# Performance work log

Hardware: AMD Instinct MI355X
Metric: run time of the kernel (lower is better)

## Reference

```python
import jax, jax.numpy as jnp
import numpy as np

B, L = 128, 64000
FS, STEP, NFILT, HID, HID2, OUT = 256, 200, 64, 512, 512, 10


def _ilin(lb, ub, W, b=0.0):
    # interval affine: center/radius form
    c = (lb + ub) * 0.5
    r = (ub - lb) * 0.5
    oc = c @ W + b
    orr = r @ jnp.abs(W)
    return oc - orr, oc + orr


def _imul(al, au, bl, bu):
    # interval product: extremes over 4 corner products
    p = jnp.stack([al * bl, al * bu, au * bl, au * bu])
    return p.min(axis=0), p.max(axis=0)


def _cell(xl, xu, hl, hu, cl, cu, wih, whh, bias):
    # interval LSTM cell, torch gate order i,f,g,o
    gl1, gu1 = _ilin(xl, xu, wih)
    gl2, gu2 = _ilin(hl, hu, whh)
    gl = gl1 + gl2 + bias
    gu = gu1 + gu2 + bias
    il, fl, ggl, ol = jnp.split(gl, 4, axis=-1)
    iu, fu, ggu, ou = jnp.split(gu, 4, axis=-1)
    il, iu = jax.nn.sigmoid(il), jax.nn.sigmoid(iu)
    fl, fu = jax.nn.sigmoid(fl), jax.nn.sigmoid(fu)
    ggl, ggu = jnp.tanh(ggl), jnp.tanh(ggu)
    fcl, fcu = _imul(fl, fu, cl, cu)
    igl, igu = _imul(il, iu, ggl, ggu)
    ncl, ncu = fcl + igl, fcu + igu
    nhl, nhu = _imul(jax.nn.sigmoid(ol), jax.nn.sigmoid(ou), jnp.tanh(ncl), jnp.tanh(ncu))
    return nhl, nhu, ncl, ncu


def setup_inputs() -> dict:
    key = jax.random.key(0)
    ks = jax.random.split(key, 13)
    x = 0.1 * jax.random.normal(ks[0], (B, L), jnp.float32)
    eps = 0.01
    s = 0.3  # keep LSTM gates out of saturation
    return {
        "input_lb": x - eps,
        "input_ub": x + eps,
        "mtx1": jax.random.normal(ks[1], (FS, FS + 2), jnp.float32) / np.float32(np.sqrt(FS)),
        "mtx2": jax.random.uniform(ks[2], (FS + 2, NFILT), jnp.float32) / np.float32(FS + 2),
        "lin1_w": jax.random.normal(ks[3], (NFILT, HID), jnp.float32) / np.float32(np.sqrt(NFILT)),
        "lin1_b": 0.01 * jax.random.normal(ks[4], (HID,), jnp.float32),
        "w_ih0": s * jax.random.normal(ks[5], (HID, 4 * HID2), jnp.float32) / np.float32(np.sqrt(HID)),
        "w_hh0": s * jax.random.normal(ks[6], (HID2, 4 * HID2), jnp.float32) / np.float32(np.sqrt(HID2)),
        "b0": 0.01 * jax.random.normal(ks[7], (4 * HID2,), jnp.float32),
        "w_ih1": s * jax.random.normal(ks[8], (HID2, 4 * HID2), jnp.float32) / np.float32(np.sqrt(HID2)),
        "w_hh1": s * jax.random.normal(ks[9], (HID2, 4 * HID2), jnp.float32) / np.float32(np.sqrt(HID2)),
        "b1": 0.01 * jax.random.normal(ks[10], (4 * HID2,), jnp.float32),
        "lin2_w": jax.random.normal(ks[11], (HID2, OUT), jnp.float32) / np.float32(np.sqrt(HID2)),
        "lin2_b": 0.01 * jax.random.normal(ks[12], (OUT,), jnp.float32),
    }


def reference(input_lb, input_ub, mtx1, mtx2, lin1_w, lin1_b,
              w_ih0, w_hh0, b0, w_ih1, w_hh1, b1, lin2_w, lin2_b):
    Bc, Lc = input_lb.shape
    pad = jnp.zeros((Bc, STEP), input_lb.dtype)
    lb = jnp.concatenate([input_lb, pad], axis=1)
    ub = jnp.concatenate([input_ub, pad], axis=1)
    Lp = Lc + STEP
    F = (Lp - FS - 1) // STEP + 1  # frames with i + FS < Lp (break condition)
    idx = jnp.arange(F)[:, None] * STEP + jnp.arange(FS)[None, :]  # [F, FS]
    flb, fub = lb[:, idx], ub[:, idx]  # [B, F, FS]
    # pre-LSTM interval chain, vectorized over all frames
    l1l, l1u = _ilin(flb, fub, mtx1)  # [B, F, FS+2]
    a, b = l1l * l1l, l1u * l1u
    squ = jnp.maximum(a, b)
    sql = jnp.where((l1l <= 0) & (l1u >= 0), 0.0, jnp.minimum(a, b))
    l2l, l2u = _ilin(sql, squ, mtx2, 1e-10)  # mtx2 >= 0, inputs >= 0 -> lb > 0
    lgl, lgu = jnp.log(l2l), jnp.log(l2u)
    n1l, n1u = _ilin(lgl, lgu, lin1_w, lin1_b)  # [B, F, HID]
    rl, ru = jnp.maximum(n1l, 0.0), jnp.maximum(n1u, 0.0)

    H2 = w_hh0.shape[0]
    z = jnp.zeros((Bc, H2), input_lb.dtype)

    def step(carry, xs):
        h0l, h0u, c0l, c0u, h1l, h1u, c1l, c1u = carry
        xl, xu = xs
        h0l, h0u, c0l, c0u = _cell(xl, xu, h0l, h0u, c0l, c0u, w_ih0, w_hh0, b0)
        h1l, h1u, c1l, c1u = _cell(h0l, h0u, h1l, h1u, c1l, c1u, w_ih1, w_hh1, b1)
        return (h0l, h0u, c0l, c0u, h1l, h1u, c1l, c1u), None

    carry, _ = jax.lax.scan(step, (z,) * 8,
                            (jnp.swapaxes(rl, 0, 1), jnp.swapaxes(ru, 0, 1)))
    h1l, h1u = carry[4], carry[5]  # last frame, top LSTM layer
    ol, ou = _ilin(h1l, h1u, lin2_w, lin2_b)
    return jnp.stack([ol, ou])  # [2, B, OUT] logit bounds
```

## Files before the change

kernel.cpp:

```cpp
#include <hip/hip_runtime.h>
#include <hip/hip_bf16.h>
#include <math.h>

#define BATCH 128
#define LEN   64000
#define FS    256
#define STEPS 200
#define NFILT 64
#define HID   512
#define HID2  512
#define NOUT  10
#define NF    320
#define G4    2048
#define KTOT  1024
#define NBLK  256
#define HSLOT (BATCH * HID2)

typedef __bf16  bf16x8 __attribute__((ext_vector_type(8)));
typedef float   f32x4  __attribute__((ext_vector_type(4)));
typedef __hip_bfloat16 hbf;

#define ARV(b)  (128 + (b) * 16)
#define REL_(i) (128 + 4096 + (i) * 16)
#define BAR_WORDS (128 + 4096 + 128)

__device__ __forceinline__ float fsig(float x) { return 1.f / (1.f + __expf(-x)); }
__device__ __forceinline__ float ftanh(float x) { return 1.f - 2.f / (__expf(2.f * x) + 1.f); }
__device__ __forceinline__ void imulf_(float al, float au, float bl, float bu,
                                       float& lo, float& hi) {
    const float p1 = al * bl, p2 = al * bu, p3 = au * bl, p4 = au * bu;
    lo = fminf(fminf(p1, p2), fminf(p3, p4));
    hi = fmaxf(fmaxf(p1, p2), fmaxf(p3, p4));
}

__device__ __forceinline__ bf16x8 loadA16_agent(const hbf* p) {
    union { unsigned long long u[2]; bf16x8 v; } t;
    unsigned long long* q = (unsigned long long*)p;
    t.u[0] = __hip_atomic_load(q,     __ATOMIC_RELAXED, __HIP_MEMORY_SCOPE_AGENT);
    t.u[1] = __hip_atomic_load(q + 1, __ATOMIC_RELAXED, __HIP_MEMORY_SCOPE_AGENT);
    return t.v;
}
__device__ __forceinline__ unsigned ld_flag(const unsigned* p) {
    return __hip_atomic_load(p, __ATOMIC_RELAXED, __HIP_MEMORY_SCOPE_AGENT);
}
__device__ __forceinline__ void st_flag(unsigned* p, unsigned v) {
    __hip_atomic_store(p, v, __ATOMIC_RELAXED, __HIP_MEMORY_SCOPE_AGENT);
}

__global__ __launch_bounds__(256) void prep_weights_kernel(
    const float* __restrict__ wih, const float* __restrict__ whh,
    hbf* __restrict__ Wt)
{
    __shared__ float tile[32][33];
    const int n0 = blockIdx.x * 32;
    const int k0 = blockIdx.y * 32;
    const int tx = threadIdx.x & 31;
    const int ty = threadIdx.x >> 5;

    for (int r = ty; r < 32; r += 8) {
        const int k = k0 + r;
        const float* src = (k < HID) ? (wih + (size_t)k * G4)
                                     : (whh + (size_t)(k - HID) * G4);
        tile[r][tx] = src[n0 + tx];
    }
    __syncthreads();
    for (int r = ty; r < 32; r += 8) {
        const int n = n0 + r;
        Wt[(size_t)n * KTOT + k0 + tx] = __float2bfloat16(tile[tx][r]);
    }
}

__global__ __launch_bounds__(256) void prep_mtx1_kernel(
    const float* __restrict__ mtx1, hbf* __restrict__ W)
{
    __shared__ float tile[32][33];
    const int n0 = blockIdx.x * 32;
    const int k0 = blockIdx.y * 32;
    const int tx = threadIdx.x & 31;
    const int ty = threadIdx.x >> 5;

    for (int r = ty; r < 32; r += 8) {
        const int k = k0 + r;
        const int n = n0 + tx;
        tile[r][tx] = (n < FS + 2) ? mtx1[k * (FS + 2) + n] : 0.f;
    }
    __syncthreads();
    for (int r = ty; r < 32; r += 8) {
        const int n = n0 + r;
        if (n < 272)
            W[(size_t)n * 256 + k0 + tx] = __float2bfloat16(tile[tx][r]);
    }
}

#define FB_A1   0
#define FB_OUT1 35840
#define FB_S2   0
#define FB_S3   35840
#define FB_SIZE 70656

__global__ __launch_bounds__(256) void frontend2_kernel(
    const float* __restrict__ lb, const float* __restrict__ ub,
    const hbf* __restrict__ Wt1f,
    const float* __restrict__ mtx2,
    const float* __restrict__ lin1_w, const float* __restrict__ lin1_b,
    hbf* __restrict__ Xc, hbf* __restrict__ Xr)
{
    __shared__ char fbuf[FB_SIZE];
    hbf*   A1c = (hbf*)(fbuf + FB_A1);
    hbf*   A1r = (hbf*)(fbuf + FB_A1 + 16 * 264 * 2);
    float* o1C = (float*)(fbuf + FB_OUT1);
    float* o1R = (float*)(fbuf + FB_OUT1 + 16 * 272 * 4);
    float* s2c = (float*)(fbuf + FB_S2);
    float* s2r = (float*)(fbuf + FB_S2 + 16 * 258 * 4);
    float* s3c = (float*)(fbuf + FB_S3);
    float* s3r = (float*)(fbuf + FB_S3 + 16 * 64 * 4);

    const int tid = threadIdx.x;
    const int row0 = blockIdx.x * 16;

    for (int c = tid; c < 16 * 256; c += 256) {
        const int m = c >> 8, i = c & 255;
        const int rowid = row0 + m;
        const int f = rowid % NF, b = rowid / NF;
        const int pos = f * STEPS + i;
        float l = 0.f, u = 0.f;
        if (pos < LEN) {
            l = lb[(size_t)b * LEN + pos];
            u = ub[(size_t)b * LEN + pos];
        }
        A1c[m * 264 + i] = __float2bfloat16(0.5f * (l + u));
        A1r[m * 264 + i] = __float2bfloat16(0.5f * (u - l));
    }
    __syncthreads();

    {
        const int w    = tid >> 6;
        const int lane = tid & 63;
        const int op   = w & 1;
        const int nh   = w >> 1;
        const int rc   = lane & 15;
        const int gk   = lane >> 4;
        const unsigned amask = op ? 0x7FFF7FFFu : 0xFFFFFFFFu;
        const hbf* ap = (op ? A1r : A1c) + rc * 264 + 8 * gk;
        float* outp = op ? o1R : o1C;

        for (int nt = nh * 9; nt < nh * 8 + 9; ++nt) {
            f32x4 acc = {0.f, 0.f, 0.f, 0.f};
            const hbf* bp = Wt1f + (size_t)(nt * 16 + rc) * 256 + 8 * gk;
#pragma unroll
            for (int k0 = 0; k0 < 256; k0 += 32) {
                const bf16x8 afr = *(const bf16x8*)(ap + k0);
                union { bf16x8 v; unsigned u[4]; } t2;
                t2.v = *(const bf16x8*)(bp + k0);
                t2.u[0] &= amask; t2.u[1] &= amask;
                t2.u[2] &= amask; t2.u[3] &= amask;
                acc = __builtin_amdgcn_mfma_f32_16x16x32_bf16(afr, t2.v, acc, 0, 0, 0);
            }
            const int n = nt * 16 + rc;
#pragma unroll
            for (int reg = 0; reg < 4; ++reg)
                outp[(4 * gk + reg) * 272 + n] = acc[reg];
        }
    }
    __syncthreads();

    for (int c = tid; c < 16 * 258; c += 256) {
        const int m = c / 258, n = c - m * 258;
        const float oc = o1C[m * 272 + n];
        const float orr = o1R[m * 272 + n];
        const float l1l = oc - orr, l1u = oc + orr;
        const float a = l1l * l1l, bb = l1u * l1u;
        const float squ = fmaxf(a, bb);
        const float sql = (l1l <= 0.f && l1u >= 0.f) ? 0.f : fminf(a, bb);
        s2c[m * 258 + n] = 0.5f * (sql + squ);
        s2r[m * 258 + n] = 0.5f * (squ - sql);
    }
    __syncthreads();

    for (int idx = tid; idx < 16 * 64; idx += 256) {
        const int m = idx >> 6, n = idx & 63;
        float oc = 1e-10f, orr = 0.f;
#pragma unroll 4
        for (int i = 0; i < FS + 2; ++i) {
            const float w = mtx2[i * NFILT + n];
            oc  = fmaf(s2c[m * 258 + i], w, oc);
            orr = fmaf(s2r[m * 258 + i], fabsf(w), orr);
        }
        const float lgl = logf(oc - orr);
        const float lgu = logf(oc + orr);
        s3c[m * 64 + n] = 0.5f * (lgl + lgu);
        s3r[m * 64 + n] = 0.5f * (lgu - lgl);
    }
    __syncthreads();

    for (int idx = tid; idx < 16 * 512; idx += 256) {
        const int m = idx >> 9, j = idx & 511;
        float oc = lin1_b[j], orr = 0.f;
#pragma unroll 4
        for (int i = 0; i < NFILT; ++i) {
            const float w = lin1_w[i * HID + j];
            oc  = fmaf(s3c[m * 64 + i], w, oc);
            orr = fmaf(s3r[m * 64 + i], fabsf(w), orr);
        }
        const float n1l = oc - orr, n1u = oc + orr;
        const float rl = fmaxf(n1l, 0.f), ru = fmaxf(n1u, 0.f);
        const int rowid = row0 + m;
        const int f = rowid % NF, b = rowid / NF;
        const size_t o = ((size_t)f * BATCH + b) * HID + j;
        Xc[o] = __float2bfloat16(0.5f * (rl + ru));
        Xr[o] = __float2bfloat16(0.5f * (ru - rl));
    }
}

__device__ __forceinline__ void gbar(unsigned* bar, unsigned gen,
                                     int bid, int tid) {
    __builtin_amdgcn_s_waitcnt(0);
    __syncthreads();
    if (bid == 0) {
        if (tid != 0) {
            while (ld_flag(&bar[ARV(tid)]) < gen)
                __builtin_amdgcn_s_sleep(1);
        }
        __syncthreads();
        if (tid < 8) st_flag(&bar[REL_(tid)], gen);
    } else {
        if (tid == 0) {
            st_flag(&bar[ARV(bid)], gen);
            while (ld_flag(&bar[REL_(bid & 7)]) < gen)
                __builtin_amdgcn_s_sleep(4);
        }
        asm volatile("" ::: "memory");
    }
    __syncthreads();
}

__device__ __forceinline__ void cell_elem(
    const float C[4], const float R[4], const float bs[4],
    float& cl_r, float& cu_r, float& nhl, float& nhu)
{
    float gl[4], gu[4];
#pragma unroll
    for (int g = 0; g < 4; ++g) {
        gl[g] = C[g] - R[g] + bs[g];
        gu[g] = C[g] + R[g] + bs[g];
    }
    const float il = fsig(gl[0]), iu = fsig(gu[0]);
    const float fl = fsig(gl[1]), fu = fsig(gu[1]);
    const float ggl = ftanh(gl[2]), ggu = ftanh(gu[2]);
    const float ol = fsig(gl[3]), ou = fsig(gu[3]);

    float fcl, fcu, igl, igu;
    imulf_(fl, fu, cl_r, cu_r, fcl, fcu);
    imulf_(il, iu, ggl, ggu, igl, igu);
    const float ncl = fcl + igl, ncu = fcu + igu;
    cl_r = ncl; cu_r = ncu;
    imulf_(ol, ou, ftanh(ncl), ftanh(ncu), nhl, nhu);
}

#define GEMM_HALF(KBASE, MASKED)                                               \
    _Pragma("unroll")                                                          \
    for (int kk = 0; kk < 16; ++kk) {                                          \
        const int KK = (KBASE) + kk;                                           \
        _Pragma("unroll")                                                      \
        for (int g = 0; g < 4; ++g) {                                          \
            union { bf16x8 v; unsigned u[4]; } t2;                             \
            t2.v = *(const bf16x8*)&Wlds[(size_t)(((g << 5) | KK) * 64 + lane) * 8]; \
            if (MASKED) {                                                      \
                t2.u[0] &= 0x7FFF7FFFu; t2.u[1] &= 0x7FFF7FFFu;                \
                t2.u[2] &= 0x7FFF7FFFu; t2.u[3] &= 0x7FFF7FFFu;                \
            }                                                                  \
            acc[g] = __builtin_amdgcn_mfma_f32_16x16x32_bf16(af[kk], t2.v, acc[g], 0, 0, 0); \
        }                                                                      \
    }

#define LOADA16(PTR)                                                           \
    _Pragma("unroll")                                                          \
    for (int i = 0; i < 16; ++i) af[i] = *(const bf16x8*)((PTR) + 32 * i);

#define POLL_GROUP(BASE, TGT)                                                  \
    if (tid < 64) {                                                            \
        const unsigned* pp = &lflags[((BASE) + (tid & 31)) * 16];              \
        for (;;) {                                                             \
            const unsigned v = ld_flag(pp);                                    \
            if (__all((int)v >= (TGT))) break;                                 \
            __builtin_amdgcn_s_sleep(1);                                       \
        }                                                                      \
    }                                                                          \
    __syncthreads();

__global__ __launch_bounds__(256, 1) void lstm_persistent(
    const hbf* Xc, const hbf* Xr,
    hbf* Ring1C, hbf* Ring1R,
    const hbf* __restrict__ Wt0, const hbf* __restrict__ Wt1,
    const float* __restrict__ b0, const float* __restrict__ b1,
    hbf* __restrict__ Ring0C, hbf* __restrict__ Ring0R,
    const hbf* __restrict__ Zbuf,
    hbf* __restrict__ H1c0, hbf* __restrict__ H1r0,
    hbf* __restrict__ H1c1, hbf* __restrict__ H1r1,
    float* __restrict__ h1l, float* __restrict__ h1u,
    unsigned* __restrict__ bar, unsigned* __restrict__ tkt,
    unsigned* __restrict__ lflags)
{
    const int tid = threadIdx.x;
    const int bid = blockIdx.x;

    __shared__ unsigned s_info, s_map;
    __shared__ int s_fast;
    __shared__ hbf   Wlds[4 * 32 * 64 * 8];
    __shared__ float red[2][2][4][64][4];
    __shared__ unsigned short houtC[32][16], houtR[32][16];

    if (tid == 0) {
        unsigned xcc;
        asm volatile("s_getreg_b32 %0, hwreg(HW_REG_XCC_ID)" : "=s"(xcc));
        xcc &= 7u;
        const unsigned slot = __hip_atomic_fetch_add(
            &tkt[xcc * 16], 1u, __ATOMIC_RELAXED, __HIP_MEMORY_SCOPE_AGENT);
        s_info = (xcc << 16) | slot;
    }
    gbar(bar, 1, bid, tid);
    if (tid == 0) {
        unsigned cnt[8]; bool ok = true;
        for (int y = 0; y < 8; ++y) {
            cnt[y] = ld_flag(&tkt[y * 16]);
            ok = ok && (cnt[y] == 32u);
        }
        const unsigned xcc = s_info >> 16, slot = s_info & 0xffffu;
        unsigned rank;
        if (ok) rank = xcc * 32u + slot;
        else { rank = slot; for (unsigned y = 0; y < xcc; ++y) rank += cnt[y]; }
        s_map = rank; s_fast = ok ? 1 : 0;
    }
    __syncthreads();

    const unsigned rank = s_map;
    const bool fast = (s_fast != 0);
    int layer, mgrp, jslot;
    if (fast) { layer = (rank >> 5) & 1; mgrp = rank >> 6; jslot = rank & 31; }
    else      { layer = rank >> 7; mgrp = (rank >> 5) & 3; jslot = rank & 31; }
    const int m0 = mgrp * 32;
    const int j0 = jslot * 16;
    const int lfbase  = layer * 128 + mgrp * 32;
    const int l0fbase = mgrp * 32;
    const int myLf = lfbase + jslot;

    {
        const hbf* Wt = layer ? Wt1 : Wt0;
        for (int c = tid; c < 8192; c += 256) {
            const int g  = c >> 11;
            const int kk = (c >> 6) & 31;
            const int l6 = c & 63;
            const int n  = g * HID2 + j0 + (l6 & 15);
            const int k  = kk * 32 + (l6 >> 4) * 8;
            *(ulonglong2*)&Wlds[(size_t)c * 8] =
                *(const ulonglong2*)(Wt + (size_t)n * KTOT + k);
        }
    }

    const int w    = tid >> 6;
    const int lane = tid & 63;
    const int op   = w & 1;
    const int mh   = w >> 1;
    const int rc   = lane & 15;
    const int gk   = lane >> 4;
    const int aoff = (m0 + mh * 16 + rc) * 512 + 8 * gk;

    hbf* H1cb[2] = { H1c0, H1c1 };
    hbf* H1rb[2] = { H1r0, H1r1 };

    const int mm  = tid >> 4;
    const int cj  = tid & 15;
    const int ll  = ((mm >> 2) << 4) | cj;
    const int rr  = mm & 3;
    const int idx0 = (m0 + mm) * HID2 + j0 + cj;
    const int idx1 = idx0 + 16 * HID2;
    const float* bias = layer ? b1 : b0;
    float bs[4];
#pragma unroll
    for (int g = 0; g < 4; ++g) bs[g] = bias[g * HID2 + j0 + cj];

    const int st_arr = tid >> 7;
    const int st_row = (tid >> 2) & 31;
    const int st_q   = tid & 3;
    const size_t st_off = (size_t)(m0 + st_row) * 512 + j0 + st_q * 4;

    float cAl = 0.f, cAu = 0.f, cBl = 0.f, cBu = 0.f;

    __syncthreads();

    bf16x8 xf[16];
    if (layer == 0) {
        const hbf* p = (op ? Xr : Xc) + aoff;
        bf16x8* af = xf;
        LOADA16(p)
    }

    for (int t = 0; t < NF; ++t) {
        const int wslot = t & 1, rslot = wslot ^ 1;
        f32x4 acc[4] = {f32x4{0,0,0,0}, f32x4{0,0,0,0},
                        f32x4{0,0,0,0}, f32x4{0,0,0,0}};

        if (layer == 0) {
            {
                bf16x8* af = xf;
                if (op) { GEMM_HALF(0, 1) } else { GEMM_HALF(0, 0) }
                const int tn = (t + 1 < NF) ? (t + 1) : t;
                const hbf* p = (op ? Xr : Xc) + (size_t)tn * HSLOT + aoff;
                LOADA16(p)
            }
            POLL_GROUP(lfbase, t)
            {
                const int pt = (t == 0) ? NF : t - 1;
                const hbf* p = (op ? Ring0R : Ring0C) + (size_t)pt * HSLOT + aoff;
                bf16x8 af[16];
                LOADA16(p)
                if (op) { GEMM_HALF(16, 1) } else { GEMM_HALF(16, 0) }
            }
        } else {
            POLL_GROUP(lfbase, t)
            {
                bf16x8 af[16];
                if (fast) {
                    const hbf* p = (t == 0) ? (Zbuf + aoff)
                        : ((op ? (const hbf*)Ring1R : (const hbf*)Ring1C)
                           + (size_t)(t - 1) * HSLOT + aoff);
                    LOADA16(p)
                } else {
                    const hbf* p = (op ? H1rb[rslot] : H1cb[rslot]) + aoff;
#pragma unroll
                    for (int i = 0; i < 16; ++i) af[i] = loadA16_agent(p + 32 * i);
                }
                if (op) { GEMM_HALF(16, 1) } else { GEMM_HALF(16, 0) }
            }
            POLL_GROUP(l0fbase, t + 1)
            {
                const hbf* p = (op ? Ring0R : Ring0C) + (size_t)t * HSLOT + aoff;
                bf16x8 af[16];
                LOADA16(p)
                if (op) { GEMM_HALF(0, 1) } else { GEMM_HALF(0, 0) }
            }
        }

#pragma unroll
        for (int g = 0; g < 4; ++g)
            *((f32x4*)&red[op][mh][g][lane][0]) = acc[g];
        __syncthreads();

        {
            float C0[4], R0[4], C1[4], R1[4];
#pragma unroll
            for (int g = 0; g < 4; ++g) {
                C0[g] = red[0][0][g][ll][rr];
                R0[g] = red[1][0][g][ll][rr];
                C1[g] = red[0][1][g][ll][rr];
                R1[g] = red[1][1][g][ll][rr];
            }
            const bool writeF = (layer == 1) && (t == NF - 1);

            float nhl, nhu;
            cell_elem(C0, R0, bs, cAl, cAu, nhl, nhu);
            {
                const __hip_bfloat16 hc = __float2bfloat16(0.5f * (nhl + nhu));
                const __hip_bfloat16 hr = __float2bfloat16(0.5f * (nhu - nhl));
                houtC[mm][cj] = *(const unsigned short*)&hc;
                houtR[mm][cj] = *(const unsigned short*)&hr;
            }
            if (writeF) { h1l[idx0] = nhl; h1u[idx0] = nhu; }

            cell_elem(C1, R1, bs, cBl, cBu, nhl, nhu);
            {
                const __hip_bfloat16 hc = __float2bfloat16(0.5f * (nhl + nhu));
                const __hip_bfloat16 hr = __float2bfloat16(0.5f * (nhu - nhl));
                houtC[mm + 16][cj] = *(const unsigned short*)&hc;
                houtR[mm + 16][cj] = *(const unsigned short*)&hr;
            }
            if (writeF) { h1l[idx1] = nhl; h1u[idx1] = nhu; }
        }
        __syncthreads();

        {
            hbf *dstC, *dstR;
            if (layer == 0) {
                dstC = Ring0C + (size_t)t * HSLOT;
                dstR = Ring0R + (size_t)t * HSLOT;
            } else if (fast) {
                dstC = Ring1C + (size_t)t * HSLOT;
                dstR = Ring1R + (size_t)t * HSLOT;
            } else {
                dstC = H1cb[wslot];
                dstR = H1rb[wslot];
            }
            const unsigned long long* src = (const unsigned long long*)
                &(st_arr ? houtR : houtC)[st_row][st_q * 4];
            unsigned long long* dst = (unsigned long long*)
                ((st_arr ? dstR : dstC) + st_off);
            __hip_atomic_store(dst, *src, __ATOMIC_RELAXED,
                               __HIP_MEMORY_SCOPE_AGENT);
        }

        __builtin_amdgcn_s_waitcnt(0);
        __syncthreads();
        if (tid == 0)
            st_flag(&lflags[myLf * 16], (unsigned)(t + 1));
    }
}

__global__ __launch_bounds__(64) void final_kernel(
    const float* __restrict__ h1l, const float* __restrict__ h1u,
    const float* __restrict__ w, const float* __restrict__ bias,
    float* __restrict__ out)
{
    const int b = blockIdx.x;
    const int j = threadIdx.x;
    if (j < NOUT) {
        float oc = bias[j], orr = 0.f;
        for (int i = 0; i < HID2; ++i) {
            const float lo = h1l[(size_t)b * HID2 + i];
            const float hi = h1u[(size_t)b * HID2 + i];
            const float wv = w[i * NOUT + j];
            oc  = fmaf(0.5f * (lo + hi), wv, oc);
            orr = fmaf(0.5f * (hi - lo), fabsf(wv), orr);
        }
        out[b * NOUT + j] = oc - orr;
        out[BATCH * NOUT + b * NOUT + j] = oc + orr;
    }
}

extern "C" void kernel_launch(void* const* d_in, const int* in_sizes, int n_in,
                              void* d_out, int out_size, void* d_ws, size_t ws_size,
                              hipStream_t stream)
{
    const float* input_lb = (const float*)d_in[0];
    const float* input_ub = (const float*)d_in[1];
    const float* mtx1     = (const float*)d_in[2];
    const float* mtx2     = (const float*)d_in[3];
    const float* lin1_w   = (const float*)d_in[4];
    const float* lin1_b   = (const float*)d_in[5];
    const float* w_ih0    = (const float*)d_in[6];
    const float* w_hh0    = (const float*)d_in[7];
    const float* b0       = (const float*)d_in[8];
    const float* w_ih1    = (const float*)d_in[9];
    const float* w_hh1    = (const float*)d_in[10];
    const float* b1       = (const float*)d_in[11];
    const float* lin2_w   = (const float*)d_in[12];
    const float* lin2_b   = (const float*)d_in[13];
    float* out = (float*)d_out;

    char* ws = (char*)d_ws;
    size_t off = 0;
    hbf* Xc = (hbf*)(ws + off); off += (size_t)NF * HSLOT * 2;
    hbf* Xr = (hbf*)(ws + off); off += (size_t)NF * HSLOT * 2;
    hbf* Wt0 = (hbf*)(ws + off); off += (size_t)G4 * KTOT * 2;
    hbf* Wt1 = (hbf*)(ws + off); off += (size_t)G4 * KTOT * 2;
    hbf* Wt1f = (hbf*)(ws + off); off += (size_t)272 * 256 * 2;
    hbf* Ring0C = (hbf*)(ws + off); off += (size_t)(NF + 1) * HSLOT * 2;
    hbf* Ring0R = (hbf*)(ws + off); off += (size_t)(NF + 1) * HSLOT * 2;

    char* zbase = ws + off;
    hbf* Zbuf = (hbf*)(ws + off); off += (size_t)HSLOT * 2;
    hbf* H1c0 = (hbf*)(ws + off); off += (size_t)HSLOT * 2;
    hbf* H1r0 = (hbf*)(ws + off); off += (size_t)HSLOT * 2;
    hbf* H1c1 = (hbf*)(ws + off); off += (size_t)HSLOT * 2;
    hbf* H1r1 = (hbf*)(ws + off); off += (size_t)HSLOT * 2;
    unsigned* lflags = (unsigned*)(ws + off); off += (size_t)256 * 16 * 4;
    unsigned* tkt    = (unsigned*)(ws + off); off += (size_t)8 * 16 * 4;
    unsigned* bar    = (unsigned*)(ws + off); off += (size_t)BAR_WORDS * 4;
    const size_t zbytes = (size_t)((ws + off) - zbase);
    float* h1l = (float*)(ws + off); off += (size_t)HSLOT * 4;
    float* h1u = (float*)(ws + off); off += (size_t)HSLOT * 4;

    hipMemsetAsync(zbase, 0, zbytes, stream);
    hipMemsetAsync(Ring0C + (size_t)NF * HSLOT, 0, (size_t)HSLOT * 2, stream);
    hipMemsetAsync(Ring0R + (size_t)NF * HSLOT, 0, (size_t)HSLOT * 2, stream);

    {
        const dim3 pgrid(G4 / 32, KTOT / 32);
        prep_weights_kernel<<<pgrid, 256, 0, stream>>>(w_ih0, w_hh0, Wt0);
        prep_weights_kernel<<<pgrid, 256, 0, stream>>>(w_ih1, w_hh1, Wt1);
        prep_mtx1_kernel<<<dim3(9, 8), 256, 0, stream>>>(mtx1, Wt1f);
    }

    frontend2_kernel<<<(BATCH * NF) / 16, 256, 0, stream>>>(
        input_lb, input_ub, Wt1f, mtx2, lin1_w, lin1_b, Xc, Xr);

    lstm_persistent<<<NBLK, 256, 0, stream>>>(
        Xc, Xr, Xc, Xr, Wt0, Wt1, b0, b1,
        Ring0C, Ring0R, Zbuf,
        H1c0, H1r0, H1c1, H1r1,
        h1l, h1u, bar, tkt, lflags);

    final_kernel<<<BATCH, 64, 0, stream>>>(h1l, h1u, lin2_w, lin2_b, out);
}
```

Before: 3.448 ms.

## Move lin1 interval matmul to MFMA and restructure frontend with 512 threads

Replaces the scalar FMA loop for the lin1 interval affine layer with bf16 MFMA tiles, using a new prep kernel that transposes lin1_w to bf16. The block size goes from 256 to 512 threads, the mtx2 stage computes lower and upper bounds directly (mtx2 is nonnegative) from bf16 squared bounds, and shared memory is compacted. The aim is to cut scalar ALU time in the frontend, at the cost of bf16 precision loss in the squared values and log-feature intermediates.

```diff
diff --git a/kernel.cpp b/kernel.cpp
--- a/kernel.cpp
+++ b/kernel.cpp
@@ -92,44 +92,63 @@
     }
 }
 
-#define FB_A1   0
-#define FB_OUT1 35840
-#define FB_S2   0
-#define FB_S3   35840
-#define FB_SIZE 70656
-
-__global__ __launch_bounds__(256) void frontend2_kernel(
+__global__ __launch_bounds__(256) void prep_lin1_kernel(
+    const float* __restrict__ lin1_w, hbf* __restrict__ W)
+{
+    __shared__ float tile[32][33];
+    const int n0 = blockIdx.x * 32;
+    const int k0 = blockIdx.y * 32;
+    const int tx = threadIdx.x & 31;
+    const int ty = threadIdx.x >> 5;
+
+    for (int r = ty; r < 32; r += 8)
+        tile[r][tx] = lin1_w[(size_t)(k0 + r) * HID + n0 + tx];
+    __syncthreads();
+    for (int r = ty; r < 32; r += 8)
+        W[(size_t)(n0 + r) * 64 + k0 + tx] = __float2bfloat16(tile[tx][r]);
+}
+
+#define FB_A1C  0
+#define FB_A1R  8704
+#define FB_O1C  17408
+#define FB_O1R  34816
+#define FB_S3C  52224
+#define FB_S3R  54272
+#define FB_SIZE 56320
+
+__global__ __launch_bounds__(512) void frontend3_kernel(
     const float* __restrict__ lb, const float* __restrict__ ub,
     const hbf* __restrict__ Wt1f,
     const float* __restrict__ mtx2,
-    const float* __restrict__ lin1_w, const float* __restrict__ lin1_b,
+    const hbf* __restrict__ Wt3f,
+    const float* __restrict__ lin1_b,
     hbf* __restrict__ Xc, hbf* __restrict__ Xr)
 {
     __shared__ char fbuf[FB_SIZE];
-    hbf*   A1c = (hbf*)(fbuf + FB_A1);
-    hbf*   A1r = (hbf*)(fbuf + FB_A1 + 16 * 264 * 2);
-    float* o1C = (float*)(fbuf + FB_OUT1);
-    float* o1R = (float*)(fbuf + FB_OUT1 + 16 * 272 * 4);
-    float* s2c = (float*)(fbuf + FB_S2);
-    float* s2r = (float*)(fbuf + FB_S2 + 16 * 258 * 4);
-    float* s3c = (float*)(fbuf + FB_S3);
-    float* s3r = (float*)(fbuf + FB_S3 + 16 * 64 * 4);
-
-    const int tid = threadIdx.x;
+    hbf*   A1c = (hbf*)(fbuf + FB_A1C);
+    hbf*   A1r = (hbf*)(fbuf + FB_A1R);
+    float* o1C = (float*)(fbuf + FB_O1C);
+    float* o1R = (float*)(fbuf + FB_O1R);
+    hbf*   SQL = A1c;
+    hbf*   SQU = A1r;
+    hbf*   s3c = (hbf*)(fbuf + FB_S3C);
+    hbf*   s3r = (hbf*)(fbuf + FB_S3R);
+
+    const int tid  = threadIdx.x;
     const int row0 = blockIdx.x * 16;
-
-    for (int c = tid; c < 16 * 256; c += 256) {
+    const int b    = row0 / NF;
+    const int f0   = row0 % NF;
+
+    for (int c = tid; c < 16 * 256; c += 512) {
         const int m = c >> 8, i = c & 255;
-        const int rowid = row0 + m;
-        const int f = rowid % NF, b = rowid / NF;
-        const int pos = f * STEPS + i;
+        const int pos = (f0 + m) * STEPS + i;
         float l = 0.f, u = 0.f;
         if (pos < LEN) {
             l = lb[(size_t)b * LEN + pos];
             u = ub[(size_t)b * LEN + pos];
         }
-        A1c[m * 264 + i] = __float2bfloat16(0.5f * (l + u));
-        A1r[m * 264 + i] = __float2bfloat16(0.5f * (u - l));
+        A1c[m * 272 + i] = __float2bfloat16(0.5f * (l + u));
+        A1r[m * 272 + i] = __float2bfloat16(0.5f * (u - l));
     }
     __syncthreads();
 
@@ -141,10 +160,11 @@
         const int rc   = lane & 15;
         const int gk   = lane >> 4;
         const unsigned amask = op ? 0x7FFF7FFFu : 0xFFFFFFFFu;
-        const hbf* ap = (op ? A1r : A1c) + rc * 264 + 8 * gk;
+        const hbf* ap = (op ? A1r : A1c) + rc * 272 + 8 * gk;
         float* outp = op ? o1R : o1C;
-
-        for (int nt = nh * 9; nt < nh * 8 + 9; ++nt) {
+        const int nt0 = nh * 4, nt1 = (nh == 3) ? 17 : nh * 4 + 4;
+
+        for (int nt = nt0; nt < nt1; ++nt) {
             f32x4 acc = {0.f, 0.f, 0.f, 0.f};
             const hbf* bp = Wt1f + (size_t)(nt * 16 + rc) * 256 + 8 * gk;
 #pragma unroll
@@ -164,7 +184,7 @@
     }
     __syncthreads();
 
-    for (int c = tid; c < 16 * 258; c += 256) {
+    for (int c = tid; c < 16 * 258; c += 512) {
         const int m = c / 258, n = c - m * 258;
         const float oc = o1C[m * 272 + n];
         const float orr = o1R[m * 272 + n];
@@ -172,43 +192,65 @@
         const float a = l1l * l1l, bb = l1u * l1u;
         const float squ = fmaxf(a, bb);
         const float sql = (l1l <= 0.f && l1u >= 0.f) ? 0.f : fminf(a, bb);
-        s2c[m * 258 + n] = 0.5f * (sql + squ);
-        s2r[m * 258 + n] = 0.5f * (squ - sql);
-    }
-    __syncthreads();
-
-    for (int idx = tid; idx < 16 * 64; idx += 256) {
+        SQL[m * 272 + n] = __float2bfloat16(sql);
+        SQU[m * 272 + n] = __float2bfloat16(squ);
+    }
+    __syncthreads();
+
+    for (int idx = tid; idx < 16 * 64; idx += 512) {
         const int m = idx >> 6, n = idx & 63;
-        float oc = 1e-10f, orr = 0.f;
-#pragma unroll 4
-        for (int i = 0; i < FS + 2; ++i) {
+        float l2l = 1e-10f, l2u = 1e-10f;
+#pragma unroll 2
+        for (int i = 0; i < 258; ++i) {
             const float w = mtx2[i * NFILT + n];
-            oc  = fmaf(s2c[m * 258 + i], w, oc);
-            orr = fmaf(s2r[m * 258 + i], fabsf(w), orr);
-        }
-        const float lgl = logf(oc - orr);
-        const float lgu = logf(oc + orr);
-        s3c[m * 64 + n] = 0.5f * (lgl + lgu);
-        s3r[m * 64 + n] = 0.5f * (lgu - lgl);
-    }
-    __syncthreads();
-
-    for (int idx = tid; idx < 16 * 512; idx += 256) {
-        const int m = idx >> 9, j = idx & 511;
-        float oc = lin1_b[j], orr = 0.f;
-#pragma unroll 4
-        for (int i = 0; i < NFILT; ++i) {
-            const float w = lin1_w[i * HID + j];
-            oc  = fmaf(s3c[m * 64 + i], w, oc);
-            orr = fmaf(s3r[m * 64 + i], fabsf(w), orr);
-        }
-        const float n1l = oc - orr, n1u = oc + orr;
-        const float rl = fmaxf(n1l, 0.f), ru = fmaxf(n1u, 0.f);
-        const int rowid = row0 + m;
-        const int f = rowid % NF, b = rowid / NF;
-        const size_t o = ((size_t)f * BATCH + b) * HID + j;
-        Xc[o] = __float2bfloat16(0.5f * (rl + ru));
-        Xr[o] = __float2bfloat16(0.5f * (ru - rl));
+            l2l = fmaf(__bfloat162float(SQL[m * 272 + i]), w, l2l);
+            l2u = fmaf(__bfloat162float(SQU[m * 272 + i]), w, l2u);
+        }
+        const float lgl = logf(l2l);
+        const float lgu = logf(l2u);
+        s3c[m * 64 + n] = __float2bfloat16(0.5f * (lgl + lgu));
+        s3r[m * 64 + n] = __float2bfloat16(0.5f * (lgu - lgl));
+    }
+    __syncthreads();
+
+    {
+        const int w    = tid >> 6;
+        const int lane = tid & 63;
+        const int rc   = lane & 15;
+        const int gk   = lane >> 4;
+        const hbf* apc = s3c + rc * 64 + 8 * gk;
+        const hbf* apr = s3r + rc * 64 + 8 * gk;
+
+        for (int nt = w * 4; nt < w * 4 + 4; ++nt) {
+            f32x4 accC = {0.f, 0.f, 0.f, 0.f};
+            f32x4 accR = {0.f, 0.f, 0.f, 0.f};
+            const hbf* bp = Wt3f + (size_t)(nt * 16 + rc) * 64 + 8 * gk;
+#pragma unroll
+            for (int k0 = 0; k0 < 64; k0 += 32) {
+                const bf16x8 ac = *(const bf16x8*)(apc + k0);
+                const bf16x8 ar = *(const bf16x8*)(apr + k0);
+                union { bf16x8 v; unsigned u[4]; } tw, ta;
+                tw.v = *(const bf16x8*)(bp + k0);
+                ta.v = tw.v;
+                ta.u[0] &= 0x7FFF7FFFu; ta.u[1] &= 0x7FFF7FFFu;
+                ta.u[2] &= 0x7FFF7FFFu; ta.u[3] &= 0x7FFF7FFFu;
+                accC = __builtin_amdgcn_mfma_f32_16x16x32_bf16(ac, tw.v, accC, 0, 0, 0);
+                accR = __builtin_amdgcn_mfma_f32_16x16x32_bf16(ar, ta.v, accR, 0, 0, 0);
+            }
+            const int n = nt * 16 + rc;
+            const float bn = lin1_b[n];
+#pragma unroll
+            for (int reg = 0; reg < 4; ++reg) {
+                const int m = 4 * gk + reg;
+                const float oc = accC[reg] + bn;
+                const float orr = accR[reg];
+                const float n1l = oc - orr, n1u = oc + orr;
+                const float rl = fmaxf(n1l, 0.f), ru = fmaxf(n1u, 0.f);
+                const size_t o = ((size_t)(f0 + m) * BATCH + b) * HID + n;
+                Xc[o] = __float2bfloat16(0.5f * (rl + ru));
+                Xr[o] = __float2bfloat16(0.5f * (ru - rl));
+            }
+        }
     }
 }
 
@@ -553,6 +595,7 @@
     hbf* Wt0 = (hbf*)(ws + off); off += (size_t)G4 * KTOT * 2;
     hbf* Wt1 = (hbf*)(ws + off); off += (size_t)G4 * KTOT * 2;
     hbf* Wt1f = (hbf*)(ws + off); off += (size_t)272 * 256 * 2;
+    hbf* Wt3f = (hbf*)(ws + off); off += (size_t)512 * 64 * 2;
     hbf* Ring0C = (hbf*)(ws + off); off += (size_t)(NF + 1) * HSLOT * 2;
     hbf* Ring0R = (hbf*)(ws + off); off += (size_t)(NF + 1) * HSLOT * 2;
 
@@ -578,10 +621,11 @@
         prep_weights_kernel<<<pgrid, 256, 0, stream>>>(w_ih0, w_hh0, Wt0);
         prep_weights_kernel<<<pgrid, 256, 0, stream>>>(w_ih1, w_hh1, Wt1);
         prep_mtx1_kernel<<<dim3(9, 8), 256, 0, stream>>>(mtx1, Wt1f);
-    }
-
-    frontend2_kernel<<<(BATCH * NF) / 16, 256, 0, stream>>>(
-        input_lb, input_ub, Wt1f, mtx2, lin1_w, lin1_b, Xc, Xr);
+        prep_lin1_kernel<<<dim3(16, 2), 256, 0, stream>>>(lin1_w, Wt3f);
+    }
+
+    frontend3_kernel<<<(BATCH * NF) / 16, 512, 0, stream>>>(
+        input_lb, input_ub, Wt1f, mtx2, Wt3f, lin1_b, Xc, Xr);
 
     lstm_persistent<<<NBLK, 256, 0, stream>>>(
         Xc, Xr, Xc, Xr, Wt0, Wt1, b0, b1,
```

Measured after the change: 2.911 ms. 15.6% less time.
